# Kernel optimization log

Hardware: AMD Instinct MI355X
Metric: run time of the kernel (lower is better)

The kernel has to match this reference:

```python
import jax, jax.numpy as jnp
import numpy as np

HIDDEN = 1024
NUM_HEADS = 16
HEAD = HIDDEN // NUM_HEADS
B, S = 2, 2048


def setup_inputs() -> dict:
    key = jax.random.key(0)
    ks = jax.random.split(key, 7)
    scale = 1.0 / np.sqrt(HIDDEN)
    return {
        "hidden_states": jax.random.normal(ks[0], (B, S, HIDDEN), dtype=jnp.float32),
        "Wq": jax.random.normal(ks[1], (HIDDEN, HIDDEN), dtype=jnp.float32) * scale,
        "bq": jax.random.normal(ks[2], (HIDDEN,), dtype=jnp.float32) * 0.01,
        "Wk": jax.random.normal(ks[3], (HIDDEN, HIDDEN), dtype=jnp.float32) * scale,
        "bk": jax.random.normal(ks[4], (HIDDEN,), dtype=jnp.float32) * 0.01,
        "Wv": jax.random.normal(ks[5], (HIDDEN, HIDDEN), dtype=jnp.float32) * scale,
        "bv": jax.random.normal(ks[6], (HIDDEN,), dtype=jnp.float32) * 0.01,
    }


def _split_heads(x):
    b, s, _ = x.shape
    return x.reshape(b, s, NUM_HEADS, HEAD).transpose(0, 2, 1, 3)  # [B,H,S,D]


def reference(hidden_states, Wq, bq, Wk, bk, Wv, bv):
    # Linear projections (dropout is inference no-op)
    Q = _split_heads(hidden_states @ Wq + bq)
    K = _split_heads(hidden_states @ Wk + bk)
    V = _split_heads(hidden_states @ Wv + bv)
    scores = jnp.einsum("bhqd,bhkd->bhqk", Q, K) / np.sqrt(HEAD).astype(np.float32)
    probs = jax.nn.softmax(scores, axis=-1)
    context = jnp.einsum("bhqk,bhkd->bhqd", probs, V)  # [B,H,S,D]
    return context.transpose(0, 2, 1, 3).reshape(B, S, HIDDEN)
```

## Files before the change

kernel.cpp:

```cpp
#include <hip/hip_runtime.h>
#include <hip/hip_bf16.h>

typedef __bf16 bf16_t;
typedef __bf16 bf16x4v __attribute__((ext_vector_type(4)));
typedef __bf16 bf16x8 __attribute__((ext_vector_type(8)));
typedef float f32x4 __attribute__((ext_vector_type(4)));
typedef float f32x16 __attribute__((ext_vector_type(16)));
typedef unsigned short u16;
typedef unsigned int u32;
typedef u16 u16x8 __attribute__((ext_vector_type(8)));

#define HIDDEN 1024
#define NHEAD 16
#define HEADD 64
#define BATCH 2
#define SEQ 2048
#define TOKENS (BATCH*SEQ)

#define Z16 {0.f,0.f,0.f,0.f,0.f,0.f,0.f,0.f,0.f,0.f,0.f,0.f,0.f,0.f,0.f,0.f}
#define M12F -12.0f
#define M16 {M12F,M12F,M12F,M12F,M12F,M12F,M12F,M12F,M12F,M12F,M12F,M12F,M12F,M12F,M12F,M12F}

__global__ __launch_bounds__(256) void k_convert_x(const float* __restrict__ x,
                                                   bf16_t* __restrict__ xb) {
  int i = (blockIdx.x * 256 + threadIdx.x) * 4;
  float4 v = *(const float4*)(x + i);
  bf16x4v o;
  o[0] = (bf16_t)v.x; o[1] = (bf16_t)v.y; o[2] = (bf16_t)v.z; o[3] = (bf16_t)v.w;
  *(bf16x4v*)(xb + i) = o;
}

__global__ __launch_bounds__(256) void k_transpose_w(const float* __restrict__ Wq,
                                                     const float* __restrict__ Wk,
                                                     const float* __restrict__ Wv,
                                                     bf16_t* __restrict__ wt) {
  int mat = blockIdx.z;
  const float* W = (mat == 0) ? Wq : (mat == 1 ? Wk : Wv);
  bf16_t* dst = wt + (size_t)mat * HIDDEN * HIDDEN;
  __shared__ float tile[32][33];
  int k0 = blockIdx.x * 32, n0 = blockIdx.y * 32;
  int tc = threadIdx.x & 31, tr = threadIdx.x >> 5;
#pragma unroll
  for (int r = 0; r < 32; r += 8)
    tile[tr + r][tc] = W[(size_t)(k0 + tr + r) * HIDDEN + n0 + tc];
  __syncthreads();
#pragma unroll
  for (int r = 0; r < 32; r += 8)
    dst[(size_t)(n0 + tr + r) * HIDDEN + k0 + tc] = (bf16_t)tile[tc][tr + r];
}

__global__ __launch_bounds__(256) void k_gemm_qkv(
    const bf16_t* __restrict__ xb, const bf16_t* __restrict__ wt,
    const float* __restrict__ bq, const float* __restrict__ bk,
    const float* __restrict__ bv, bf16_t* __restrict__ Qo,
    bf16_t* __restrict__ Ko, bf16_t* __restrict__ Vo) {
  __shared__ bf16x8 As[2][4 * 128];
  __shared__ bf16x8 Bs[2][4 * 128];
  int t = threadIdx.x;
  int wave = t >> 6, lane = t & 63;
  int m0 = blockIdx.x * 128;
  int nb = blockIdx.y;
  int mat = nb >> 3;
  int n0 = (nb & 7) * 128;
  const bf16_t* Wmat = wt + (size_t)mat * HIDDEN * HIDDEN;
  const float* bias = (mat == 0) ? bq : (mat == 1 ? bk : bv);
  bf16_t* dst = (mat == 0) ? Qo : (mat == 1 ? Ko : Vo);

  int wm = wave >> 1, wn = wave & 1;
  int lrow = lane & 15;
  int lc = lane >> 4;

  f32x4 acc[4][4];
#pragma unroll
  for (int a = 0; a < 4; ++a)
#pragma unroll
    for (int b = 0; b < 4; ++b) acc[a][b] = (f32x4){0.f, 0.f, 0.f, 0.f};

  bf16x8 ra[2], rb[2];
  auto load_tiles = [&](int kt) {
    int k0 = kt * 32;
#pragma unroll
    for (int u = 0; u < 2; ++u) {
      int id = t + u * 256;
      int row = id >> 2, c = id & 3;
      ra[u] = *(const bf16x8*)(xb + (size_t)(m0 + row) * HIDDEN + k0 + c * 8);
      rb[u] = *(const bf16x8*)(Wmat + (size_t)(n0 + row) * HIDDEN + k0 + c * 8);
    }
  };
  auto store_tiles = [&](int buf) {
#pragma unroll
    for (int u = 0; u < 2; ++u) {
      int id = t + u * 256;
      int row = id >> 2, c = id & 3;
      As[buf][c * 128 + (row ^ c)] = ra[u];
      Bs[buf][c * 128 + (row ^ c)] = rb[u];
    }
  };

  load_tiles(0);
  store_tiles(0);
  __syncthreads();
  const int NT = HIDDEN / 32;
  int cur = 0;
  for (int kt = 0; kt < NT; ++kt) {
    if (kt + 1 < NT) load_tiles(kt + 1);
    bf16x8 af[4], bfr[4];
#pragma unroll
    for (int fm = 0; fm < 4; ++fm)
      af[fm] = As[cur][lc * 128 + ((wm * 64 + fm * 16 + lrow) ^ lc)];
#pragma unroll
    for (int fn = 0; fn < 4; ++fn)
      bfr[fn] = Bs[cur][lc * 128 + ((wn * 64 + fn * 16 + lrow) ^ lc)];
#pragma unroll
    for (int fm = 0; fm < 4; ++fm)
#pragma unroll
      for (int fn = 0; fn < 4; ++fn)
        acc[fm][fn] = __builtin_amdgcn_mfma_f32_16x16x32_bf16(
            af[fm], bfr[fn], acc[fm][fn], 0, 0, 0);
    if (kt + 1 < NT) store_tiles(cur ^ 1);
    __syncthreads();
    cur ^= 1;
  }

  float scale = (mat == 0) ? 0.18033688011112042f : 1.0f;
#pragma unroll
  for (int fm = 0; fm < 4; ++fm) {
#pragma unroll
    for (int fn = 0; fn < 4; ++fn) {
      int n = n0 + wn * 64 + fn * 16 + (lane & 15);
      float bval = bias[n];
      int h = n >> 6, d = n & 63;
      int mbase = m0 + wm * 64 + fm * 16 + (lane >> 4) * 4;
      int b = mbase >> 11, s = mbase & 2047;
      if (mat == 2) {
        bf16x4v pk;
#pragma unroll
        for (int j = 0; j < 4; ++j) pk[j] = (bf16_t)(acc[fm][fn][j] + bval);
        *(bf16x4v*)(dst + ((size_t)(b * NHEAD + h) * HEADD + d) * SEQ + s) = pk;
      } else {
#pragma unroll
        for (int j = 0; j < 4; ++j) {
          float v = (acc[fm][fn][j] + bval) * scale;
          dst[((size_t)(b * NHEAD + h) * SEQ + (s + j)) * HEADD + d] = (bf16_t)v;
        }
      }
    }
  }
}

__device__ __forceinline__ void gload16(const void* g, void* l) {
  __builtin_amdgcn_global_load_lds((const __attribute__((address_space(1))) u32*)g,
                                   (__attribute__((address_space(3))) u32*)l, 16, 0, 0);
}

__global__ __launch_bounds__(512, 4) void k_attn(const bf16_t* __restrict__ Q,
                                                 const bf16_t* __restrict__ K,
                                                 const bf16_t* __restrict__ Vt,
                                                 float* __restrict__ out) {
  __shared__ __align__(16) char smem[66560];
  const int t = threadIdx.x;
  const int w = t >> 6, l = t & 63;
  const int g = w >> 2, wg = w & 3;
  const int hi = l >> 5;
  const int l31 = l & 31;
  const int lx = l & 7;

  const int n_hw = blockIdx.x + 16 * blockIdx.y;
  const int work = (n_hw & 7) * 64 + (n_hw >> 3);
  const int qt = work & 15;
  const int bh = work >> 4;
  const int b = bh >> 4, h = bh & 15;
  const char* Kp = (const char*)(K + (size_t)bh * SEQ * HEADD) + (size_t)g * 1024 * 128;
  const char* Vp = (const char*)(Vt + (size_t)bh * HEADD * SEQ) + (size_t)g * 1024 * 2;
  const bf16_t* Qp = Q + (size_t)bh * SEQ * HEADD;

  const int q0 = qt * 128 + wg * 32;

  bf16x8 qa[4];
#pragma unroll
  for (int ds = 0; ds < 4; ++ds)
    qa[ds] = *(const bf16x8*)(Qp + (size_t)(q0 + l31) * HEADD + ds * 16 + hi * 8);

  f32x16 o0 = Z16, o1 = Z16;
  float l_run = 0.f;

  char* gK = smem + g * 32768;
  char* gV = gK + 16384;
  const int srow = wg * 16 + (l >> 3);
  const int sg = lx ^ (l >> 3);

  auto stage = [&](int tile, int buf) {
#pragma unroll
    for (int s = 0; s < 2; ++s) {
      int row = srow + 8 * s;
      gload16(Kp + (size_t)(tile * 64 + row) * 128 + sg * 16,
              gK + buf * 8192 + wg * 2048 + s * 1024);
      gload16(Vp + (size_t)row * (SEQ * 2) + tile * 128 + sg * 16,
              gV + buf * 8192 + wg * 2048 + s * 1024);
    }
  };

  stage(0, 0);
  __syncthreads();

  int roff0[4], roff1[4];
#pragma unroll
  for (int ds = 0; ds < 4; ++ds) {
    roff0[ds] = l31 * 128 + ((2 * ds + hi) ^ lx) * 16;
    roff1[ds] = (32 + l31) * 128 + ((2 * ds + hi) ^ lx) * 16;
  }

  int cur = 0;
  for (int r = 0; r < 16; ++r) {
    if (r < 15) stage(r + 1, cur ^ 1);
    const char* Kc = gK + cur * 8192;
    const char* Vc = gV + cur * 8192;

    f32x16 s0 = M16, s1 = M16;
    __builtin_amdgcn_s_setprio(1);
#pragma unroll
    for (int ds = 0; ds < 4; ++ds) {
      bf16x8 kf0 = *(const bf16x8*)(Kc + roff0[ds]);
      s0 = __builtin_amdgcn_mfma_f32_32x32x16_bf16(kf0, qa[ds], s0, 0, 0, 0);
      bf16x8 kf1 = *(const bf16x8*)(Kc + roff1[ds]);
      s1 = __builtin_amdgcn_mfma_f32_32x32x16_bf16(kf1, qa[ds], s1, 0, 0, 0);
    }
    __builtin_amdgcn_s_setprio(0);

#pragma unroll
    for (int i = 0; i < 16; ++i) {
      s0[i] = __builtin_amdgcn_exp2f(s0[i]);
      s1[i] = __builtin_amdgcn_exp2f(s1[i]);
    }
    {
      float ta[16];
#pragma unroll
      for (int i = 0; i < 16; ++i) ta[i] = s0[i] + s1[i];
#pragma unroll
      for (int i = 0; i < 8; ++i) ta[i] += ta[i + 8];
#pragma unroll
      for (int i = 0; i < 4; ++i) ta[i] += ta[i + 4];
      l_run += (ta[0] + ta[1]) + (ta[2] + ta[3]);
    }

    bf16x8 pf[4];
    {
      u32 u[16];
#pragma unroll
      for (int i = 0; i < 8; ++i) {
        union { bf16_t h[2]; u32 ww; } c0, c1;
        c0.h[0] = (bf16_t)s0[2 * i]; c0.h[1] = (bf16_t)s0[2 * i + 1];
        c1.h[0] = (bf16_t)s1[2 * i]; c1.h[1] = (bf16_t)s1[2 * i + 1];
        u[i] = c0.ww; u[8 + i] = c1.ww;
      }
#pragma unroll
      for (int gg = 0; gg < 4; ++gg) {
        u32 a0 = u[4 * gg + 0], b0 = u[4 * gg + 2];
        u32 a1 = u[4 * gg + 1], b1 = u[4 * gg + 3];
        asm("v_permlane32_swap_b32 %0, %1" : "+v"(a0), "+v"(b0));
        asm("v_permlane32_swap_b32 %0, %1" : "+v"(a1), "+v"(b1));
        union { u32 wv[4]; bf16x8 v; } fu;
        fu.wv[0] = a0; fu.wv[1] = a1; fu.wv[2] = b0; fu.wv[3] = b1;
        pf[gg] = fu.v;
      }
    }

    __builtin_amdgcn_s_setprio(1);
#pragma unroll
    for (int kblk = 0; kblk < 4; ++kblk) {
      bf16x8 vf0 = *(const bf16x8*)(Vc + roff0[kblk]);
      o0 = __builtin_amdgcn_mfma_f32_32x32x16_bf16(vf0, pf[kblk], o0, 0, 0, 0);
      bf16x8 vf1 = *(const bf16x8*)(Vc + roff1[kblk]);
      o1 = __builtin_amdgcn_mfma_f32_32x32x16_bf16(vf1, pf[kblk], o1, 0, 0, 0);
    }
    __builtin_amdgcn_s_setprio(0);
    __syncthreads();
    cur ^= 1;
  }

  float l_half = l_run + __shfl_xor(l_run, 32);
  float* OL = (float*)(smem + g * 32768);
  const int orow = wg * 32 + l31;
#pragma unroll
  for (int j = 0; j < 16; ++j) {
    int dv0 = (j & 3) + 8 * (j >> 2) + 4 * hi;
    OL[orow * 64 + ((dv0 + orow) & 63)] = o0[j];
    int dv1 = 32 + dv0;
    OL[orow * 64 + ((dv1 + orow) & 63)] = o1[j];
  }
  float* LL = (float*)(smem + 65536);
  if (hi == 0) LL[g * 128 + orow] = l_half;
  __syncthreads();
  {
    int ql = t >> 2;
    int dvb = (t & 3) * 16;
    float inv = 1.0f / (LL[ql] + LL[128 + ql]);
    const float* A0 = (const float*)smem;
    const float* B0 = (const float*)(smem + 32768);
    float* op = out + ((size_t)b * SEQ + qt * 128 + ql) * HIDDEN + h * HEADD + dvb;
#pragma unroll
    for (int g4 = 0; g4 < 4; ++g4) {
      f32x4 v4;
#pragma unroll
      for (int e = 0; e < 4; ++e) {
        int dv = dvb + g4 * 4 + e;
        int idx = ql * 64 + ((dv + ql) & 63);
        v4[e] = (A0[idx] + B0[idx]) * inv;
      }
      *(f32x4*)(op + g4 * 4) = v4;
    }
  }
}

extern "C" void kernel_launch(void* const* d_in, const int* in_sizes, int n_in,
                              void* d_out, int out_size, void* d_ws, size_t ws_size,
                              hipStream_t stream) {
  const float* hs = (const float*)d_in[0];
  const float* Wq = (const float*)d_in[1];
  const float* bq = (const float*)d_in[2];
  const float* Wk = (const float*)d_in[3];
  const float* bk = (const float*)d_in[4];
  const float* Wv = (const float*)d_in[5];
  const float* bv = (const float*)d_in[6];
  float* out = (float*)d_out;
  char* ws = (char*)d_ws;

  const size_t SZ_X = (size_t)TOKENS * HIDDEN * 2;
  const size_t SZ_W = (size_t)3 * HIDDEN * HIDDEN * 2;
  const size_t SZ_P = (size_t)TOKENS * HIDDEN * 2;
  bf16_t* Xb = (bf16_t*)ws;
  bf16_t* Wt = (bf16_t*)(ws + SZ_X);
  bf16_t* Qb = (bf16_t*)(ws + SZ_X + SZ_W);
  bf16_t* Kb = (bf16_t*)(ws + SZ_X + SZ_W + SZ_P);
  bf16_t* Vb = (bf16_t*)(ws + SZ_X + SZ_W + 2 * SZ_P);

  k_convert_x<<<4096, 256, 0, stream>>>(hs, Xb);
  k_transpose_w<<<dim3(32, 32, 3), 256, 0, stream>>>(Wq, Wk, Wv, Wt);
  k_gemm_qkv<<<dim3(32, 24), 256, 0, stream>>>(Xb, Wt, bq, bk, bv, Qb, Kb, Vb);
  k_attn<<<dim3(16, 32), 512, 0, stream>>>(Qb, Kb, Vb, out);
}
```

Before: 107.6 us.

## Fuse fp32-to-bf16 input conversion into QKV GEMM and load V directly

Removes the separate conversion kernel, so the QKV GEMM reads fp32 hidden states and converts them to bf16 while loading tiles. This saves one launch and a full write/read pass over the bf16 copy, but doubles the global bytes the GEMM reads for the A operand. The attention kernel also stops staging V tiles through shared memory and loads V fragments straight from global memory into registers each iteration, which halves the LDS footprint per group. The trade-off is uncoalesced, per-lane global loads on the critical path in place of the shared-memory double buffer.

```diff
diff --git a/kernel.cpp b/kernel.cpp
--- a/kernel.cpp
+++ b/kernel.cpp
@@ -20,15 +20,6 @@
 #define Z16 {0.f,0.f,0.f,0.f,0.f,0.f,0.f,0.f,0.f,0.f,0.f,0.f,0.f,0.f,0.f,0.f}
 #define M12F -12.0f
 #define M16 {M12F,M12F,M12F,M12F,M12F,M12F,M12F,M12F,M12F,M12F,M12F,M12F,M12F,M12F,M12F,M12F}
-
-__global__ __launch_bounds__(256) void k_convert_x(const float* __restrict__ x,
-                                                   bf16_t* __restrict__ xb) {
-  int i = (blockIdx.x * 256 + threadIdx.x) * 4;
-  float4 v = *(const float4*)(x + i);
-  bf16x4v o;
-  o[0] = (bf16_t)v.x; o[1] = (bf16_t)v.y; o[2] = (bf16_t)v.z; o[3] = (bf16_t)v.w;
-  *(bf16x4v*)(xb + i) = o;
-}
 
 __global__ __launch_bounds__(256) void k_transpose_w(const float* __restrict__ Wq,
                                                      const float* __restrict__ Wk,
@@ -50,7 +41,7 @@
 }
 
 __global__ __launch_bounds__(256) void k_gemm_qkv(
-    const bf16_t* __restrict__ xb, const bf16_t* __restrict__ wt,
+    const float* __restrict__ hs, const bf16_t* __restrict__ wt,
     const float* __restrict__ bq, const float* __restrict__ bk,
     const float* __restrict__ bv, bf16_t* __restrict__ Qo,
     bf16_t* __restrict__ Ko, bf16_t* __restrict__ Vo) {
@@ -83,7 +74,13 @@
     for (int u = 0; u < 2; ++u) {
       int id = t + u * 256;
       int row = id >> 2, c = id & 3;
-      ra[u] = *(const bf16x8*)(xb + (size_t)(m0 + row) * HIDDEN + k0 + c * 8);
+      const float* ap = hs + (size_t)(m0 + row) * HIDDEN + k0 + c * 8;
+      float4 f0 = *(const float4*)(ap);
+      float4 f1 = *(const float4*)(ap + 4);
+      bf16x8 v;
+      v[0] = (bf16_t)f0.x; v[1] = (bf16_t)f0.y; v[2] = (bf16_t)f0.z; v[3] = (bf16_t)f0.w;
+      v[4] = (bf16_t)f1.x; v[5] = (bf16_t)f1.y; v[6] = (bf16_t)f1.z; v[7] = (bf16_t)f1.w;
+      ra[u] = v;
       rb[u] = *(const bf16x8*)(Wmat + (size_t)(n0 + row) * HIDDEN + k0 + c * 8);
     }
   };
@@ -184,8 +181,7 @@
   f32x16 o0 = Z16, o1 = Z16;
   float l_run = 0.f;
 
-  char* gK = smem + g * 32768;
-  char* gV = gK + 16384;
+  char* gK = smem + g * 16384;
   const int srow = wg * 16 + (l >> 3);
   const int sg = lx ^ (l >> 3);
 
@@ -195,8 +191,6 @@
       int row = srow + 8 * s;
       gload16(Kp + (size_t)(tile * 64 + row) * 128 + sg * 16,
               gK + buf * 8192 + wg * 2048 + s * 1024);
-      gload16(Vp + (size_t)row * (SEQ * 2) + tile * 128 + sg * 16,
-              gV + buf * 8192 + wg * 2048 + s * 1024);
     }
   };
 
@@ -209,12 +203,12 @@
     roff0[ds] = l31 * 128 + ((2 * ds + hi) ^ lx) * 16;
     roff1[ds] = (32 + l31) * 128 + ((2 * ds + hi) ^ lx) * 16;
   }
+  const char* vlane = Vp + l31 * (SEQ * 2) + hi * 16;
 
   int cur = 0;
   for (int r = 0; r < 16; ++r) {
     if (r < 15) stage(r + 1, cur ^ 1);
     const char* Kc = gK + cur * 8192;
-    const char* Vc = gV + cur * 8192;
 
     f32x16 s0 = M16, s1 = M16;
     __builtin_amdgcn_s_setprio(1);
@@ -226,6 +220,14 @@
       s1 = __builtin_amdgcn_mfma_f32_32x32x16_bf16(kf1, qa[ds], s1, 0, 0, 0);
     }
     __builtin_amdgcn_s_setprio(0);
+
+    const char* vb = vlane + r * 128;
+    bf16x8 vf0[4], vf1[4];
+#pragma unroll
+    for (int kblk = 0; kblk < 4; ++kblk) {
+      vf0[kblk] = *(const bf16x8*)(vb + kblk * 32);
+      vf1[kblk] = *(const bf16x8*)(vb + 32 * (SEQ * 2) + kblk * 32);
+    }
 
 #pragma unroll
     for (int i = 0; i < 16; ++i) {
@@ -268,10 +270,8 @@
     __builtin_amdgcn_s_setprio(1);
 #pragma unroll
     for (int kblk = 0; kblk < 4; ++kblk) {
-      bf16x8 vf0 = *(const bf16x8*)(Vc + roff0[kblk]);
-      o0 = __builtin_amdgcn_mfma_f32_32x32x16_bf16(vf0, pf[kblk], o0, 0, 0, 0);
-      bf16x8 vf1 = *(const bf16x8*)(Vc + roff1[kblk]);
-      o1 = __builtin_amdgcn_mfma_f32_32x32x16_bf16(vf1, pf[kblk], o1, 0, 0, 0);
+      o0 = __builtin_amdgcn_mfma_f32_32x32x16_bf16(vf0[kblk], pf[kblk], o0, 0, 0, 0);
+      o1 = __builtin_amdgcn_mfma_f32_32x32x16_bf16(vf1[kblk], pf[kblk], o1, 0, 0, 0);
     }
     __builtin_amdgcn_s_setprio(0);
     __syncthreads();
@@ -328,14 +328,12 @@
   const size_t SZ_X = (size_t)TOKENS * HIDDEN * 2;
   const size_t SZ_W = (size_t)3 * HIDDEN * HIDDEN * 2;
   const size_t SZ_P = (size_t)TOKENS * HIDDEN * 2;
-  bf16_t* Xb = (bf16_t*)ws;
   bf16_t* Wt = (bf16_t*)(ws + SZ_X);
   bf16_t* Qb = (bf16_t*)(ws + SZ_X + SZ_W);
   bf16_t* Kb = (bf16_t*)(ws + SZ_X + SZ_W + SZ_P);
   bf16_t* Vb = (bf16_t*)(ws + SZ_X + SZ_W + 2 * SZ_P);
 
-  k_convert_x<<<4096, 256, 0, stream>>>(hs, Xb);
   k_transpose_w<<<dim3(32, 32, 3), 256, 0, stream>>>(Wq, Wk, Wv, Wt);
-  k_gemm_qkv<<<dim3(32, 24), 256, 0, stream>>>(Xb, Wt, bq, bk, bv, Qb, Kb, Vb);
+  k_gemm_qkv<<<dim3(32, 24), 256, 0, stream>>>(hs, Wt, bq, bk, bv, Qb, Kb, Vb);
   k_attn<<<dim3(16, 32), 512, 0, stream>>>(Qb, Kb, Vb, out);
 }
```

New measurement: 196.3 us. +82.5%, slower.
